# Kernel tuning notes

Measured on AMD Instinct MI355X. Metric: run time of the kernel, lower is better.

The kernel has to match this reference:

```python
import jax, jax.numpy as jnp
import numpy as np

SPECIES = [1, 6, 7, 8]
N_SPECIES = len(SPECIES)
MAX_Z = max(SPECIES) + 1  # 9
N_IN = 256
N_HIDDEN = 512
N_OUT = 1
N_ATOMS = 65536


def setup_inputs() -> dict:
    key = jax.random.key(0)
    ks = jax.random.split(key, 9)
    x = jax.random.normal(ks[0], (N_ATOMS, N_IN), dtype=jnp.float32)
    z = jax.random.randint(ks[1], (N_ATOMS,), 0, MAX_Z)
    s = 0.05
    # Stacked per-species MLP parameters: [S, ...]
    W1 = jax.random.normal(ks[2], (N_SPECIES, N_HIDDEN, N_IN), dtype=jnp.float32) * s
    b1 = jax.random.normal(ks[3], (N_SPECIES, N_HIDDEN), dtype=jnp.float32) * s
    W2 = jax.random.normal(ks[4], (N_SPECIES, N_HIDDEN, N_HIDDEN), dtype=jnp.float32) * s
    b2 = jax.random.normal(ks[5], (N_SPECIES, N_HIDDEN), dtype=jnp.float32) * s
    W3 = jax.random.normal(ks[6], (N_SPECIES, N_OUT, N_HIDDEN), dtype=jnp.float32) * s
    b3 = jax.random.normal(ks[7], (N_SPECIES, N_OUT), dtype=jnp.float32) * s
    # One-hot embedding table [MAX_Z, N_SPECIES]: row Z has 1.0 at its species slot
    E = np.zeros((MAX_Z, N_SPECIES), dtype=np.float32)
    for idx, Z in enumerate(SPECIES):
        E[Z, idx] = 1.0
    E = jnp.asarray(E)
    return {"x": x, "z": z, "W1": W1, "b1": b1, "W2": W2, "b2": b2,
            "W3": W3, "b3": b3, "E": E}


def reference(x, z, W1, b1, W2, b2, W3, b3, E):
    # Every atom runs through all species MLPs (dense, O(N*S)), as in the original.
    # h1: [N, S, H]
    h1 = jnp.tanh(jnp.einsum('ni,shi->nsh', x, W1) + b1[None])
    h2 = jnp.tanh(jnp.einsum('nsh,sgh->nsg', h1, W2) + b2[None])
    # out_s: [N, S, n_out] -> [N, S*n_out] (n_out == 1 -> [N, S])
    out_s = (jnp.einsum('nsh,soh->nso', h2, W3) + b3[None]).reshape(x.shape[0], -1)
    gate = E[z]  # [N, S] embedding lookup (one-hot hard routing)
    return jnp.sum(out_s * gate, axis=1)  # [N]
```

## Files before the change

### kernel.cpp

```cpp
#include <hip/hip_runtime.h>

typedef __attribute__((ext_vector_type(8))) short bf16x8;
typedef __attribute__((ext_vector_type(4))) float f32x4;
typedef __attribute__((ext_vector_type(2))) unsigned int u32x2;
typedef unsigned short us;

#define NATOMS 65536
#define NIN 256
#define NHID 512
#define TM 64
#define LDBX 528
#define LDBH 1040

__device__ __forceinline__ us f2b(float f) {
    union { float f; unsigned int u; } a; a.f = f;
    unsigned int r = a.u + 0x7FFFu + ((a.u >> 16) & 1u);
    return (us)(r >> 16);
}
__device__ __forceinline__ float fast_tanh(float v) {
    float t = __builtin_amdgcn_exp2f(v * 2.88539008f);
    float r = __builtin_amdgcn_rcpf(t + 1.f);
    return __builtin_fmaf(-2.f, r, 1.f);
}
__device__ __forceinline__ unsigned cvt_pk(float lo, float hi) {
    unsigned p;
    asm("v_cvt_pk_bf16_f32 %0, %1, %2" : "=v"(p) : "v"(lo), "v"(hi));
    return p;
}

__global__ void cvt_kernel(const float* __restrict__ W1, const float* __restrict__ W2,
                           const float* __restrict__ W3,
                           us* __restrict__ W1p, us* __restrict__ W2p,
                           us* __restrict__ W3b) {
    int i = blockIdx.x * blockDim.x + threadIdx.x;
    if (i < 65536) {
        int s = i >> 14, rem = i & 16383;
        int ntile = rem >> 9, r2 = rem & 511;
        int kstep = r2 >> 6, lane = r2 & 63;
        int n = ntile * 16 + (lane & 15);
        int k = kstep * 32 + ((lane >> 4) << 3);
        const float* src = W1 + ((size_t)(s * NHID + n) * NIN + k);
        us p[8];
#pragma unroll
        for (int j = 0; j < 8; ++j) p[j] = f2b(src[j]);
        *(uint4*)(W1p + (size_t)i * 8) = *(uint4*)p;
    }
    if (i < 131072) {
        int s = i >> 15, rem = i & 32767;
        int ntile = rem >> 10, r2 = rem & 1023;
        int kstep = r2 >> 6, lane = r2 & 63;
        int n = ntile * 16 + (lane & 15);
        int k = kstep * 32 + ((lane >> 4) << 3);
        const float* src = W2 + ((size_t)(s * NHID + n) * NHID + k);
        us p[8];
#pragma unroll
        for (int j = 0; j < 8; ++j) p[j] = f2b(src[j]);
        *(uint4*)(W2p + (size_t)i * 8) = *(uint4*)p;
    }
    if (i < 2048) W3b[i] = f2b(W3[i]);
}

__global__ __launch_bounds__(1024) void compact_kernel(
    const int* __restrict__ z, int* __restrict__ cnt,
    int* __restrict__ lists, float* __restrict__ out) {
    __shared__ int lcnt[4];
    __shared__ int gbase[4];
    __shared__ int wbase[16][4];

    int tid = threadIdx.x;
    int wv = tid >> 6;
    int lane = tid & 63;
    if (tid < 4) lcnt[tid] = 0;
    __syncthreads();

    int i = blockIdx.x * 1024 + tid;
    int zz = z[i];
    int s = (zz == 1) ? 0 : (zz == 6) ? 1 : (zz == 7) ? 2 : (zz == 8) ? 3 : -1;
    if (s < 0) out[i] = 0.f;

    int prefix = 0;
#pragma unroll
    for (int sp = 0; sp < 4; ++sp) {
        unsigned long long m = __ballot(s == sp);
        if (m) {
            int c = __popcll(m);
            int leader = __ffsll((long long)m) - 1;
            if (lane == leader) wbase[wv][sp] = atomicAdd(&lcnt[sp], c);
            if (s == sp) prefix = __popcll(m & ((1ull << lane) - 1ull));
        }
    }
    __syncthreads();
    if (tid < 4) gbase[tid] = atomicAdd(&cnt[tid], lcnt[tid]);
    __syncthreads();

    if (s >= 0) lists[s * NATOMS + gbase[s] + wbase[wv][s] + prefix] = i;
}

template<int K, int LDB>
__device__ __forceinline__ void gemm4(const char* lds, const us* Wp,
                                      int lane, int wtile, f32x4 acc[4][4]) {
    constexpr int KS = K / 32;
    const us* wp[4];
#pragma unroll
    for (int nt = 0; nt < 4; ++nt)
        wp[nt] = Wp + (((size_t)(wtile + nt) * KS) * 64 + lane) * 8;
    int aoff[4];
#pragma unroll
    for (int mt = 0; mt < 4; ++mt)
        aoff[mt] = (mt * 16 + (lane & 15)) * LDB + (((lane >> 4) << 3) << 1);

    bf16x8 a[2][4], b[2][4];
#pragma unroll
    for (int mt = 0; mt < 4; ++mt) a[0][mt] = *(const bf16x8*)(lds + aoff[mt]);
#pragma unroll
    for (int nt = 0; nt < 4; ++nt) b[0][nt] = *(const bf16x8*)wp[nt];

#pragma unroll
    for (int i = 0; i < KS; ++i) {
        const int cur = i & 1, nxt = cur ^ 1;
        if (i + 1 < KS) {
#pragma unroll
            for (int mt = 0; mt < 4; ++mt)
                a[nxt][mt] = *(const bf16x8*)(lds + aoff[mt] + (i + 1) * 64);
#pragma unroll
            for (int nt = 0; nt < 4; ++nt)
                b[nxt][nt] = *(const bf16x8*)(wp[nt] + (i + 1) * 512);
        }
#pragma unroll
        for (int nt = 0; nt < 4; ++nt)
#pragma unroll
            for (int mt = 0; mt < 4; ++mt)
                acc[mt][nt] = __builtin_amdgcn_mfma_f32_16x16x32_bf16(a[cur][mt], b[cur][nt], acc[mt][nt], 0, 0, 0);
    }
}

template<int LDB>
__device__ __forceinline__ void act_store(char* ldsOut, const float* __restrict__ bias,
                                          int lane, int ncb, f32x4 acc[4][4]) {
#pragma unroll
    for (int nt = 0; nt < 4; ++nt) {
        int n = ncb + nt * 16 + (lane & 15);
        float bv = bias[n];
#pragma unroll
        for (int mt = 0; mt < 4; ++mt) {
            float t0 = fast_tanh(acc[mt][nt][0] + bv);
            float t1 = fast_tanh(acc[mt][nt][1] + bv);
            float t2 = fast_tanh(acc[mt][nt][2] + bv);
            float t3 = fast_tanh(acc[mt][nt][3] + bv);
            unsigned p01 = cvt_pk(t0, t1);
            unsigned p23 = cvt_pk(t2, t3);
            int row0 = mt * 16 + ((lane >> 4) << 2);
            char* base = ldsOut + row0 * LDB + n * 2;
            *(us*)(base)           = (us)p01;
            *(us*)(base + LDB)     = (us)(p01 >> 16);
            *(us*)(base + 2 * LDB) = (us)p23;
            *(us*)(base + 3 * LDB) = (us)(p23 >> 16);
        }
    }
}

__global__ __launch_bounds__(512, 1) void mlp_kernel(
    const float* __restrict__ x, const int* __restrict__ cnt, const int* __restrict__ lists,
    const us* __restrict__ W1p, const us* __restrict__ W2p, const us* __restrict__ W3b,
    const float* __restrict__ b1, const float* __restrict__ b2, const float* __restrict__ b3,
    float* __restrict__ out) {
    int bx = blockIdx.x;
    int s = bx & 3;
    int t = bx >> 2;
    int base = t * TM;
    int n_s = cnt[s];
    if (base >= n_s) return;
    const int* list = lists + s * NATOMS;
    int cnt_t = n_s - base; if (cnt_t > TM) cnt_t = TM;

    __shared__ __align__(16) char ldsX[TM * LDBX];
    __shared__ __align__(16) char ldsH[TM * LDBH];

    int tid = threadIdx.x;
    int lane = tid & 63;
    int w = tid >> 6;
    int wtile = w * 4;
    int ncb = w * 64;

    {
        int r = tid >> 3;
        int cb = (tid & 7) * 32;
        int atom = (r < cnt_t) ? list[base + r] : -1;
        const float* xr = x + (size_t)(atom < 0 ? 0 : atom) * NIN;
#pragma unroll
        for (int j = 0; j < 8; ++j) {
            int c = cb + j * 4;
            float4 v;
            if (atom >= 0) v = *(const float4*)(xr + c);
            else v = make_float4(0.f, 0.f, 0.f, 0.f);
            u32x2 p;
            p.x = cvt_pk(v.x, v.y);
            p.y = cvt_pk(v.z, v.w);
            *(u32x2*)(ldsX + r * LDBX + c * 2) = p;
        }
    }
    __syncthreads();

    {
        f32x4 acc[4][4];
#pragma unroll
        for (int i = 0; i < 4; ++i)
#pragma unroll
            for (int j = 0; j < 4; ++j) acc[i][j] = (f32x4){0.f, 0.f, 0.f, 0.f};
        gemm4<NIN, LDBX>(ldsX, W1p + (size_t)s * NHID * NIN, lane, wtile, acc);
        act_store<LDBH>(ldsH, b1 + s * NHID, lane, ncb, acc);
    }
    __syncthreads();

    {
        f32x4 acc[4][4];
#pragma unroll
        for (int i = 0; i < 4; ++i)
#pragma unroll
            for (int j = 0; j < 4; ++j) acc[i][j] = (f32x4){0.f, 0.f, 0.f, 0.f};
        gemm4<NHID, LDBH>(ldsH, W2p + (size_t)s * NHID * NHID, lane, wtile, acc);
        __syncthreads();
        act_store<LDBH>(ldsH, b2 + s * NHID, lane, ncb, acc);
    }
    __syncthreads();

    {
        int m = tid >> 3;
        int q = tid & 7;
        const us* W3s = W3b + (size_t)s * NHID;
        float sum = 0.f;
#pragma unroll
        for (int j = 0; j < 8; ++j) {
            int hh = q * 64 + j * 8;
            bf16x8 hv = *(const bf16x8*)(ldsH + m * LDBH + hh * 2);
            bf16x8 wv = *(const bf16x8*)(W3s + hh);
#pragma unroll
            for (int e = 0; e < 8; ++e) {
                union { unsigned u; float f; } ha, wa;
                ha.u = ((unsigned)(us)hv[e]) << 16;
                wa.u = ((unsigned)(us)wv[e]) << 16;
                sum += ha.f * wa.f;
            }
        }
        sum += __shfl_xor(sum, 1);
        sum += __shfl_xor(sum, 2);
        sum += __shfl_xor(sum, 4);
        if (q == 0 && m < cnt_t) out[list[base + m]] = sum + b3[s];
    }
}

extern "C" void kernel_launch(void* const* d_in, const int* in_sizes, int n_in,
                              void* d_out, int out_size, void* d_ws, size_t ws_size,
                              hipStream_t stream) {
    const float* x  = (const float*)d_in[0];
    const int*   z  = (const int*)d_in[1];
    const float* W1 = (const float*)d_in[2];
    const float* b1 = (const float*)d_in[3];
    const float* W2 = (const float*)d_in[4];
    const float* b2 = (const float*)d_in[5];
    const float* W3 = (const float*)d_in[6];
    const float* b3 = (const float*)d_in[7];
    float* out = (float*)d_out;

    char* ws = (char*)d_ws;
    int* cnt = (int*)ws;
    int* lists = (int*)(ws + 256);
    us* W1p = (us*)(ws + 256 + (size_t)4 * NATOMS * 4);
    us* W2p = W1p + 4 * NHID * NIN;
    us* W3b = W2p + 4 * NHID * NHID;

    (void)hipMemsetAsync(cnt, 0, 16, stream);
    cvt_kernel<<<512, 256, 0, stream>>>(W1, W2, W3, W1p, W2p, W3b);
    compact_kernel<<<NATOMS / 1024, 1024, 0, stream>>>(z, cnt, lists, out);
    mlp_kernel<<<4096, 512, 0, stream>>>(x, cnt, lists, W1p, W2p, W3b, b1, b2, b3, out);
}
```

Baseline: 61.99 us.

## Reuse X buffer for hidden activations to fit two blocks per CU

Replaces the separate input and hidden LDS buffers with two equal-width buffers, storing the hidden layer split across them and reusing the input buffer for the upper half. This shrinks shared memory per block so launch bounds can request two blocks per CU, aiming to overlap phases across blocks. An extra barrier is needed after the first GEMM before overwriting inputs, and halving the register budget may cause spills.

```diff
diff --git a/kernel.cpp b/kernel.cpp
--- a/kernel.cpp
+++ b/kernel.cpp
@@ -9,8 +9,7 @@
 #define NIN 256
 #define NHID 512
 #define TM 64
-#define LDBX 528
-#define LDBH 1040
+#define LDB 528
 
 __device__ __forceinline__ us f2b(float f) {
     union { float f; unsigned int u; } a; a.f = f;
@@ -96,8 +95,8 @@
     if (s >= 0) lists[s * NATOMS + gbase[s] + wbase[wv][s] + prefix] = i;
 }
 
-template<int K, int LDB>
-__device__ __forceinline__ void gemm4(const char* lds, const us* Wp,
+template<int K>
+__device__ __forceinline__ void gemm4(const char* ldsLo, const char* ldsHi, const us* Wp,
                                       int lane, int wtile, f32x4 acc[4][4]) {
     constexpr int KS = K / 32;
     const us* wp[4];
@@ -111,7 +110,7 @@
 
     bf16x8 a[2][4], b[2][4];
 #pragma unroll
-    for (int mt = 0; mt < 4; ++mt) a[0][mt] = *(const bf16x8*)(lds + aoff[mt]);
+    for (int mt = 0; mt < 4; ++mt) a[0][mt] = *(const bf16x8*)(ldsLo + aoff[mt]);
 #pragma unroll
     for (int nt = 0; nt < 4; ++nt) b[0][nt] = *(const bf16x8*)wp[nt];
 
@@ -119,12 +118,14 @@
     for (int i = 0; i < KS; ++i) {
         const int cur = i & 1, nxt = cur ^ 1;
         if (i + 1 < KS) {
+            const int j = i + 1;
+            const char* src = (j < 8) ? (ldsLo + j * 64) : (ldsHi + (j - 8) * 64);
 #pragma unroll
             for (int mt = 0; mt < 4; ++mt)
-                a[nxt][mt] = *(const bf16x8*)(lds + aoff[mt] + (i + 1) * 64);
+                a[nxt][mt] = *(const bf16x8*)(src + aoff[mt]);
 #pragma unroll
             for (int nt = 0; nt < 4; ++nt)
-                b[nxt][nt] = *(const bf16x8*)(wp[nt] + (i + 1) * 512);
+                b[nxt][nt] = *(const bf16x8*)(wp[nt] + j * 512);
         }
 #pragma unroll
         for (int nt = 0; nt < 4; ++nt)
@@ -134,13 +135,15 @@
     }
 }
 
-template<int LDB>
-__device__ __forceinline__ void act_store(char* ldsOut, const float* __restrict__ bias,
-                                          int lane, int ncb, f32x4 acc[4][4]) {
+__device__ __forceinline__ void act_store_split(char* bufA, char* bufB,
+                                                const float* __restrict__ bias,
+                                                int lane, int ncb, f32x4 acc[4][4]) {
+    char* dstBase = (ncb < 256) ? bufA : bufB;
+    int coff = (ncb < 256) ? ncb : (ncb - 256);
 #pragma unroll
     for (int nt = 0; nt < 4; ++nt) {
-        int n = ncb + nt * 16 + (lane & 15);
-        float bv = bias[n];
+        int nl = coff + nt * 16 + (lane & 15);
+        float bv = bias[ncb + nt * 16 + (lane & 15)];
 #pragma unroll
         for (int mt = 0; mt < 4; ++mt) {
             float t0 = fast_tanh(acc[mt][nt][0] + bv);
@@ -150,7 +153,7 @@
             unsigned p01 = cvt_pk(t0, t1);
             unsigned p23 = cvt_pk(t2, t3);
             int row0 = mt * 16 + ((lane >> 4) << 2);
-            char* base = ldsOut + row0 * LDB + n * 2;
+            char* base = dstBase + row0 * LDB + nl * 2;
             *(us*)(base)           = (us)p01;
             *(us*)(base + LDB)     = (us)(p01 >> 16);
             *(us*)(base + 2 * LDB) = (us)p23;
@@ -159,7 +162,7 @@
     }
 }
 
-__global__ __launch_bounds__(512, 1) void mlp_kernel(
+__global__ __launch_bounds__(512, 2) void mlp_kernel(
     const float* __restrict__ x, const int* __restrict__ cnt, const int* __restrict__ lists,
     const us* __restrict__ W1p, const us* __restrict__ W2p, const us* __restrict__ W3b,
     const float* __restrict__ b1, const float* __restrict__ b2, const float* __restrict__ b3,
@@ -173,8 +176,8 @@
     const int* list = lists + s * NATOMS;
     int cnt_t = n_s - base; if (cnt_t > TM) cnt_t = TM;
 
-    __shared__ __align__(16) char ldsX[TM * LDBX];
-    __shared__ __align__(16) char ldsH[TM * LDBH];
+    __shared__ __align__(16) char bufA[TM * LDB];
+    __shared__ __align__(16) char bufB[TM * LDB];
 
     int tid = threadIdx.x;
     int lane = tid & 63;
@@ -196,7 +199,7 @@
             u32x2 p;
             p.x = cvt_pk(v.x, v.y);
             p.y = cvt_pk(v.z, v.w);
-            *(u32x2*)(ldsX + r * LDBX + c * 2) = p;
+            *(u32x2*)(bufB + r * LDB + c * 2) = p;
         }
     }
     __syncthreads();
@@ -207,8 +210,9 @@
         for (int i = 0; i < 4; ++i)
 #pragma unroll
             for (int j = 0; j < 4; ++j) acc[i][j] = (f32x4){0.f, 0.f, 0.f, 0.f};
-        gemm4<NIN, LDBX>(ldsX, W1p + (size_t)s * NHID * NIN, lane, wtile, acc);
-        act_store<LDBH>(ldsH, b1 + s * NHID, lane, ncb, acc);
+        gemm4<NIN>(bufB, bufB, W1p + (size_t)s * NHID * NIN, lane, wtile, acc);
+        __syncthreads();
+        act_store_split(bufA, bufB, b1 + s * NHID, lane, ncb, acc);
     }
     __syncthreads();
 
@@ -218,9 +222,9 @@
         for (int i = 0; i < 4; ++i)
 #pragma unroll
             for (int j = 0; j < 4; ++j) acc[i][j] = (f32x4){0.f, 0.f, 0.f, 0.f};
-        gemm4<NHID, LDBH>(ldsH, W2p + (size_t)s * NHID * NHID, lane, wtile, acc);
+        gemm4<NHID>(bufA, bufB, W2p + (size_t)s * NHID * NHID, lane, wtile, acc);
         __syncthreads();
-        act_store<LDBH>(ldsH, b2 + s * NHID, lane, ncb, acc);
+        act_store_split(bufA, bufB, b2 + s * NHID, lane, ncb, acc);
     }
     __syncthreads();
 
@@ -228,12 +232,14 @@
         int m = tid >> 3;
         int q = tid & 7;
         const us* W3s = W3b + (size_t)s * NHID;
+        const char* src = (q < 4) ? bufA : bufB;
+        int cbase = (q < 4) ? q * 64 : q * 64 - 256;
         float sum = 0.f;
 #pragma unroll
         for (int j = 0; j < 8; ++j) {
-            int hh = q * 64 + j * 8;
-            bf16x8 hv = *(const bf16x8*)(ldsH + m * LDBH + hh * 2);
-            bf16x8 wv = *(const bf16x8*)(W3s + hh);
+            int hh = cbase + j * 8;
+            bf16x8 hv = *(const bf16x8*)(src + m * LDB + hh * 2);
+            bf16x8 wv = *(const bf16x8*)(W3s + q * 64 + j * 8);
 #pragma unroll
             for (int e = 0; e < 8; ++e) {
                 union { unsigned u; float f; } ha, wa;
```

Result: slower. 66.35 us (+7.0%).
